# Performance work log

Measured on AMD Instinct MI355X. Metric: run time of the kernel, lower is better.

The kernel has to match this reference:

```python
import jax, jax.numpy as jnp
import numpy as np

FACTOR = 5

def setup_inputs() -> dict:
    key = jax.random.key(0)
    k1, k2, k3 = jax.random.split(key, 3)
    B, L, H, D = 4, 2048, 8, 64
    logL = int(np.ceil(np.log(L)))          # 8
    U_part = min(2 * FACTOR * logL, L)      # 80 sampled keys per query
    queries = jax.random.normal(k1, (B, L, H, D), dtype=jnp.float32)
    keys = jax.random.normal(k2, (B, L, H, D), dtype=jnp.float32)
    index_sample = jax.random.randint(k3, (L, U_part), 0, L)
    return {"queries": queries, "keys": keys, "index_sample": index_sample}

def reference(queries, keys, index_sample):
    B, L, H, D = queries.shape
    q = jnp.transpose(queries, (0, 2, 1, 3))   # [B,H,L,D]
    k = jnp.transpose(keys, (0, 2, 1, 3))      # [B,H,L,D]
    logL = int(np.ceil(np.log(L)))
    u = min(FACTOR * logL, L)                  # n_top queries

    # sample keys per query position: [B,H,L,S,D]
    K_sample = k[:, :, index_sample, :]
    # Q_i . K_sample_ij : [B,H,L,S]
    QK_sample = jnp.einsum('bhld,bhlsd->bhls', q, K_sample)
    # sparsity measure M = max - mean (mean over full L as in source)
    M = QK_sample.max(axis=-1) - QK_sample.sum(axis=-1) / L   # [B,H,L]
    _, M_top = jax.lax.top_k(M, u)                            # [B,H,u]

    # gather selected queries and compute full scores against all keys
    Q_reduce = jnp.take_along_axis(q, M_top[..., None], axis=2)  # [B,H,u,D]
    scale = 1.0 / jnp.sqrt(jnp.float32(D))
    scores = jnp.einsum('bhud,bhld->bhul', Q_reduce, k) * scale  # [B,H,u,L]
    attn = jax.nn.softmax(scores, axis=-1)

    # scatter softmaxed rows into full [B,H,L,L] attention matrix (rest zeros)
    out = jnp.zeros((B, H, L, L), dtype=attn.dtype)
    b_idx = jnp.arange(B)[:, None, None]
    h_idx = jnp.arange(H)[None, :, None]
    out = out.at[b_idx, h_idx, M_top, :].set(attn)
    return out
```

## Files before the change

### kernel.cpp

```cpp
#include <hip/hip_runtime.h>
#include <math.h>

#define NB 4
#define NL 2048
#define NH 8
#define ND 64
#define NUPART 80
#define NUTOP 40

typedef float vfloat4 __attribute__((ext_vector_type(4)));

__global__ __launch_bounds__(256) void k_compute_M(
    const float* __restrict__ q, const float* __restrict__ k,
    const int* __restrict__ idx, float* __restrict__ M)
{
    const int w    = blockIdx.x * 4 + (threadIdx.x >> 6);
    const int lane = threadIdx.x & 63;
    const int l    = w & (NL - 1);
    const int bh   = w >> 11;
    const int h    = bh & (NH - 1);
    const int b    = bh >> 3;
    const int sl   = lane >> 2;
    const int dg   = lane & 3;
    const int d0   = dg * 16;

    const float4* qv = (const float4*)(q + (((size_t)(b * NL + l) * NH + h) * ND + d0));
    const float4 q0 = qv[0], q1 = qv[1], q2 = qv[2], q3 = qv[3];

    float mx = -INFINITY, sm = 0.0f;
#pragma unroll
    for (int r = 0; r < 5; ++r) {
        const int s  = r * 16 + sl;
        const int ki = idx[l * NUPART + s];
        const float4* kv = (const float4*)(k + (((size_t)(b * NL + ki) * NH + h) * ND + d0));
        const float4 k0 = kv[0], k1 = kv[1], k2 = kv[2], k3 = kv[3];
        float p = q0.x * k0.x + q0.y * k0.y + q0.z * k0.z + q0.w * k0.w
                + q1.x * k1.x + q1.y * k1.y + q1.z * k1.z + q1.w * k1.w
                + q2.x * k2.x + q2.y * k2.y + q2.z * k2.z + q2.w * k2.w
                + q3.x * k3.x + q3.y * k3.y + q3.z * k3.z + q3.w * k3.w;
        p += __shfl_xor(p, 1);
        p += __shfl_xor(p, 2);
        mx = fmaxf(mx, p);
        sm += p;
    }
#pragma unroll
    for (int m = 4; m < 64; m <<= 1) {
        mx = fmaxf(mx, __shfl_xor(mx, m));
        sm += __shfl_xor(sm, m);
    }
    if (lane == 0) M[w] = mx - sm * (1.0f / (float)NL);
}

__global__ __launch_bounds__(256) void k_topk(
    const float* __restrict__ M, int* __restrict__ rowmap)
{
    __shared__ float sM[NL];
    __shared__ float rv[4];
    __shared__ int   ri[4];
    const int bh = blockIdx.x;
    const int t  = threadIdx.x;

    for (int j = t; j < NL; j += 256) {
        sM[j] = M[bh * NL + j];
        rowmap[bh * NL + j] = 0;
    }
    __syncthreads();

    for (int it = 0; it < NUTOP; ++it) {
        float v = -INFINITY;
        int   i = NL;
        for (int j = t; j < NL; j += 256) {
            const float m = sM[j];
            if (m > v || (m == v && j < i)) { v = m; i = j; }
        }
#pragma unroll
        for (int off = 1; off < 64; off <<= 1) {
            const float ov = __shfl_xor(v, off);
            const int   oi = __shfl_xor(i, off);
            if (ov > v || (ov == v && oi < i)) { v = ov; i = oi; }
        }
        const int wid = t >> 6;
        if ((t & 63) == 0) { rv[wid] = v; ri[wid] = i; }
        __syncthreads();
        if (t == 0) {
            for (int w2 = 1; w2 < 4; ++w2) {
                if (rv[w2] > v || (rv[w2] == v && ri[w2] < i)) { v = rv[w2]; i = ri[w2]; }
            }
            rowmap[bh * NL + i] = 1;
            sM[i] = -INFINITY;
        }
        __syncthreads();
    }
}

__global__ __launch_bounds__(256) void k_out(
    const float* __restrict__ q, const float* __restrict__ k,
    const int* __restrict__ rowmap, float* __restrict__ out)
{
    const int r   = blockIdx.x;
    const int bh  = r >> 11;
    const int row = r & (NL - 1);
    const int b   = bh >> 3;
    const int h   = bh & 7;
    const int t   = threadIdx.x;

    vfloat4* orow = (vfloat4*)(out + (size_t)r * NL);

    if (!rowmap[r]) {
        const vfloat4 z = (vfloat4)(0.0f);
        __builtin_nontemporal_store(z, orow + t);
        __builtin_nontemporal_store(z, orow + t + 256);
        return;
    }

    __shared__ float redm[4];
    __shared__ float reds[4];
    const int lane = t & 63;
    const int wid  = t >> 6;

    const float4* qv = (const float4*)(q + (((size_t)(b * NL + row)) * NH + h) * ND);
    float4 qr[16];
#pragma unroll
    for (int i = 0; i < 16; ++i) qr[i] = qv[i];

    float sc[8];
    float mx = -INFINITY;
#pragma unroll
    for (int j = 0; j < 8; ++j) {
        const int l = t + 256 * j;
        const float4* kv = (const float4*)(k + (((size_t)(b * NL + l)) * NH + h) * ND);
        float s = 0.0f;
#pragma unroll
        for (int i = 0; i < 16; ++i) {
            const float4 kk = kv[i];
            s += qr[i].x * kk.x + qr[i].y * kk.y + qr[i].z * kk.z + qr[i].w * kk.w;
        }
        sc[j] = s * 0.125f;
        mx = fmaxf(mx, sc[j]);
    }

#pragma unroll
    for (int off = 1; off < 64; off <<= 1) mx = fmaxf(mx, __shfl_xor(mx, off));
    if (lane == 0) redm[wid] = mx;
    __syncthreads();
    mx = fmaxf(fmaxf(redm[0], redm[1]), fmaxf(redm[2], redm[3]));

    float lsum = 0.0f;
#pragma unroll
    for (int j = 0; j < 8; ++j) {
        sc[j] = __expf(sc[j] - mx);
        lsum += sc[j];
    }
#pragma unroll
    for (int off = 1; off < 64; off <<= 1) lsum += __shfl_xor(lsum, off);
    if (lane == 0) reds[wid] = lsum;
    __syncthreads();
    const float inv = 1.0f / (reds[0] + reds[1] + reds[2] + reds[3]);

#pragma unroll
    for (int j = 0; j < 8; ++j) {
        __builtin_nontemporal_store(sc[j] * inv, out + (size_t)r * NL + t + 256 * j);
    }
}

extern "C" void kernel_launch(void* const* d_in, const int* in_sizes, int n_in,
                              void* d_out, int out_size, void* d_ws, size_t ws_size,
                              hipStream_t stream) {
    const float* q   = (const float*)d_in[0];
    const float* k   = (const float*)d_in[1];
    const int*   idx = (const int*)d_in[2];
    float* out = (float*)d_out;

    float* Mws    = (float*)d_ws;
    int*   rowmap = (int*)((char*)d_ws + (size_t)NB * NH * NL * 4);

    k_compute_M<<<NB * NH * NL / 4, 256, 0, stream>>>(q, k, idx, Mws);
    k_topk<<<NB * NH, 256, 0, stream>>>(Mws, rowmap);
    k_out<<<NB * NH * NL, 256, 0, stream>>>(q, k, rowmap, out);
}
```

Before: 413.0 us.

## Fuse all stages into one persistent kernel with grid barriers and overlapped zeroing

Replaces the three launches (sparsity measure, top-k, output) with a single persistent kernel of 512 blocks synchronised by atomic grid barriers. Zeroing of the large output matrix is spread across the phases: it runs alongside the M computation, and idle blocks keep zeroing during the serial top-k on the 32 (batch, head) blocks. The selected attention rows are then computed interleaved with zeroing the remaining rows. The aim is to hide the latency of the launches and of the top-k behind bandwidth-bound zero stores. The cost is barrier spin overhead, a reliance on all blocks being co-resident, and plain stores replacing the earlier nontemporal stores.

Result: slower. 446.5 us (+8.1%).

```diff
diff --git a/kernel.cpp b/kernel.cpp
--- a/kernel.cpp
+++ b/kernel.cpp
@@ -7,159 +7,203 @@
 #define ND 64
 #define NUPART 80
 #define NUTOP 40
+#define NBLK 512
+#define NROWS (NB * NH * NL)
+#define NATTN (NB * NH * NUTOP)
+#define Z1ROWS 20480
+#define Z2ROWS 2048
+#define Z3BASE (Z1ROWS + Z2ROWS)
+#define Z3ROWS (NROWS - Z3BASE)
 
 typedef float vfloat4 __attribute__((ext_vector_type(4)));
 
-__global__ __launch_bounds__(256) void k_compute_M(
+__device__ __forceinline__ void zero_row(float* __restrict__ out, int r, int t) {
+    vfloat4* o = (vfloat4*)out + (size_t)r * (NL / 4) + t;
+    const vfloat4 z = (vfloat4)(0.0f);
+    o[0]   = z;
+    o[256] = z;
+}
+
+__device__ __forceinline__ void gbar(int* cnt, int* gen, int target) {
+    __syncthreads();
+    if (threadIdx.x == 0) {
+        __threadfence();
+        if (atomicAdd(cnt, 1) == NBLK - 1) {
+            atomicExch(cnt, 0);
+            __threadfence();
+            atomicExch(gen, target);
+        } else {
+            while (__hip_atomic_load(gen, __ATOMIC_RELAXED,
+                                     __HIP_MEMORY_SCOPE_AGENT) < target) {
+                __builtin_amdgcn_s_sleep(8);
+            }
+        }
+        __threadfence();
+    }
+    __syncthreads();
+}
+
+__global__ __launch_bounds__(256, 2) void k_fused(
     const float* __restrict__ q, const float* __restrict__ k,
-    const int* __restrict__ idx, float* __restrict__ M)
-{
-    const int w    = blockIdx.x * 4 + (threadIdx.x >> 6);
-    const int lane = threadIdx.x & 63;
-    const int l    = w & (NL - 1);
-    const int bh   = w >> 11;
-    const int h    = bh & (NH - 1);
-    const int b    = bh >> 3;
-    const int sl   = lane >> 2;
-    const int dg   = lane & 3;
-    const int d0   = dg * 16;
-
-    const float4* qv = (const float4*)(q + (((size_t)(b * NL + l) * NH + h) * ND + d0));
-    const float4 q0 = qv[0], q1 = qv[1], q2 = qv[2], q3 = qv[3];
-
-    float mx = -INFINITY, sm = 0.0f;
-#pragma unroll
-    for (int r = 0; r < 5; ++r) {
-        const int s  = r * 16 + sl;
-        const int ki = idx[l * NUPART + s];
-        const float4* kv = (const float4*)(k + (((size_t)(b * NL + ki) * NH + h) * ND + d0));
-        const float4 k0 = kv[0], k1 = kv[1], k2 = kv[2], k3 = kv[3];
-        float p = q0.x * k0.x + q0.y * k0.y + q0.z * k0.z + q0.w * k0.w
-                + q1.x * k1.x + q1.y * k1.y + q1.z * k1.z + q1.w * k1.w
-                + q2.x * k2.x + q2.y * k2.y + q2.z * k2.z + q2.w * k2.w
-                + q3.x * k3.x + q3.y * k3.y + q3.z * k3.z + q3.w * k3.w;
-        p += __shfl_xor(p, 1);
-        p += __shfl_xor(p, 2);
-        mx = fmaxf(mx, p);
-        sm += p;
-    }
-#pragma unroll
-    for (int m = 4; m < 64; m <<= 1) {
-        mx = fmaxf(mx, __shfl_xor(mx, m));
-        sm += __shfl_xor(sm, m);
-    }
-    if (lane == 0) M[w] = mx - sm * (1.0f / (float)NL);
-}
-
-__global__ __launch_bounds__(256) void k_topk(
-    const float* __restrict__ M, int* __restrict__ rowmap)
+    const int* __restrict__ idx, float* __restrict__ M,
+    int* __restrict__ rowmap, int* __restrict__ Mtop,
+    int* __restrict__ bar, float* __restrict__ out)
 {
     __shared__ float sM[NL];
     __shared__ float rv[4];
     __shared__ int   ri[4];
-    const int bh = blockIdx.x;
-    const int t  = threadIdx.x;
-
-    for (int j = t; j < NL; j += 256) {
-        sM[j] = M[bh * NL + j];
-        rowmap[bh * NL + j] = 0;
-    }
-    __syncthreads();
-
-    for (int it = 0; it < NUTOP; ++it) {
-        float v = -INFINITY;
-        int   i = NL;
-        for (int j = t; j < NL; j += 256) {
-            const float m = sM[j];
-            if (m > v || (m == v && j < i)) { v = m; i = j; }
-        }
-#pragma unroll
-        for (int off = 1; off < 64; off <<= 1) {
-            const float ov = __shfl_xor(v, off);
-            const int   oi = __shfl_xor(i, off);
-            if (ov > v || (ov == v && oi < i)) { v = ov; i = oi; }
-        }
-        const int wid = t >> 6;
-        if ((t & 63) == 0) { rv[wid] = v; ri[wid] = i; }
-        __syncthreads();
-        if (t == 0) {
-            for (int w2 = 1; w2 < 4; ++w2) {
-                if (rv[w2] > v || (rv[w2] == v && ri[w2] < i)) { v = rv[w2]; i = ri[w2]; }
-            }
-            rowmap[bh * NL + i] = 1;
-            sM[i] = -INFINITY;
-        }
-        __syncthreads();
-    }
-}
-
-__global__ __launch_bounds__(256) void k_out(
-    const float* __restrict__ q, const float* __restrict__ k,
-    const int* __restrict__ rowmap, float* __restrict__ out)
-{
-    const int r   = blockIdx.x;
-    const int bh  = r >> 11;
-    const int row = r & (NL - 1);
-    const int b   = bh >> 3;
-    const int h   = bh & 7;
-    const int t   = threadIdx.x;
-
-    vfloat4* orow = (vfloat4*)(out + (size_t)r * NL);
-
-    if (!rowmap[r]) {
-        const vfloat4 z = (vfloat4)(0.0f);
-        __builtin_nontemporal_store(z, orow + t);
-        __builtin_nontemporal_store(z, orow + t + 256);
-        return;
-    }
-
     __shared__ float redm[4];
     __shared__ float reds[4];
+
+    const int t    = threadIdx.x;
+    const int bid  = blockIdx.x;
+    const int wid  = t >> 6;
     const int lane = t & 63;
-    const int wid  = t >> 6;
-
-    const float4* qv = (const float4*)(q + (((size_t)(b * NL + row)) * NH + h) * ND);
-    float4 qr[16];
-#pragma unroll
-    for (int i = 0; i < 16; ++i) qr[i] = qv[i];
-
-    float sc[8];
-    float mx = -INFINITY;
-#pragma unroll
-    for (int j = 0; j < 8; ++j) {
-        const int l = t + 256 * j;
-        const float4* kv = (const float4*)(k + (((size_t)(b * NL + l)) * NH + h) * ND);
-        float s = 0.0f;
-#pragma unroll
-        for (int i = 0; i < 16; ++i) {
-            const float4 kk = kv[i];
-            s += qr[i].x * kk.x + qr[i].y * kk.y + qr[i].z * kk.z + qr[i].w * kk.w;
-        }
-        sc[j] = s * 0.125f;
-        mx = fmaxf(mx, sc[j]);
-    }
-
-#pragma unroll
-    for (int off = 1; off < 64; off <<= 1) mx = fmaxf(mx, __shfl_xor(mx, off));
-    if (lane == 0) redm[wid] = mx;
-    __syncthreads();
-    mx = fmaxf(fmaxf(redm[0], redm[1]), fmaxf(redm[2], redm[3]));
-
-    float lsum = 0.0f;
-#pragma unroll
-    for (int j = 0; j < 8; ++j) {
-        sc[j] = __expf(sc[j] - mx);
-        lsum += sc[j];
-    }
-#pragma unroll
-    for (int off = 1; off < 64; off <<= 1) lsum += __shfl_xor(lsum, off);
-    if (lane == 0) reds[wid] = lsum;
-    __syncthreads();
-    const float inv = 1.0f / (reds[0] + reds[1] + reds[2] + reds[3]);
-
-#pragma unroll
-    for (int j = 0; j < 8; ++j) {
-        __builtin_nontemporal_store(sc[j] * inv, out + (size_t)r * NL + t + 256 * j);
+
+    {
+        const int gw = bid * 4 + wid;
+        const int sl = lane >> 2;
+        const int dg = lane & 3;
+        const int d0 = dg * 16;
+
+        for (int j = 0; j < 40; ++j) {
+            if (j < 32) {
+                const int w  = gw + 2048 * j;
+                const int l  = w & (NL - 1);
+                const int bh = w >> 11;
+                const int h  = bh & (NH - 1);
+                const int b  = bh >> 3;
+
+                const float4* qv = (const float4*)(q + (((size_t)(b * NL + l) * NH + h) * ND + d0));
+                const float4 q0 = qv[0], q1 = qv[1], q2 = qv[2], q3 = qv[3];
+
+                float mx = -INFINITY, sm = 0.0f;
+#pragma unroll
+                for (int r = 0; r < 5; ++r) {
+                    const int s  = r * 16 + sl;
+                    const int ki = idx[l * NUPART + s];
+                    const float4* kv = (const float4*)(k + (((size_t)(b * NL + ki) * NH + h) * ND + d0));
+                    const float4 k0 = kv[0], k1 = kv[1], k2 = kv[2], k3 = kv[3];
+                    float p = q0.x * k0.x + q0.y * k0.y + q0.z * k0.z + q0.w * k0.w
+                            + q1.x * k1.x + q1.y * k1.y + q1.z * k1.z + q1.w * k1.w
+                            + q2.x * k2.x + q2.y * k2.y + q2.z * k2.z + q2.w * k2.w
+                            + q3.x * k3.x + q3.y * k3.y + q3.z * k3.z + q3.w * k3.w;
+                    p += __shfl_xor(p, 1);
+                    p += __shfl_xor(p, 2);
+                    mx = fmaxf(mx, p);
+                    sm += p;
+                }
+#pragma unroll
+                for (int m = 4; m < 64; m <<= 1) {
+                    mx = fmaxf(mx, __shfl_xor(mx, m));
+                    sm += __shfl_xor(sm, m);
+                }
+                if (lane == 0) M[w] = mx - sm * (1.0f / (float)NL);
+            }
+            zero_row(out, j * NBLK + bid, t);
+        }
+    }
+
+    gbar(bar, bar + 1, 1);
+
+    if (bid < NB * NH) {
+        const int bh = bid;
+        for (int j = t; j < NL; j += 256) {
+            sM[j] = M[bh * NL + j];
+            rowmap[bh * NL + j] = 0;
+        }
+        __syncthreads();
+
+        for (int it = 0; it < NUTOP; ++it) {
+            float v = -INFINITY;
+            int   i = NL;
+            for (int j = t; j < NL; j += 256) {
+                const float m = sM[j];
+                if (m > v || (m == v && j < i)) { v = m; i = j; }
+            }
+#pragma unroll
+            for (int off = 1; off < 64; off <<= 1) {
+                const float ov = __shfl_xor(v, off);
+                const int   oi = __shfl_xor(i, off);
+                if (ov > v || (ov == v && oi < i)) { v = ov; i = oi; }
+            }
+            if ((t & 63) == 0) { rv[wid] = v; ri[wid] = i; }
+            __syncthreads();
+            if (t == 0) {
+                for (int w2 = 1; w2 < 4; ++w2) {
+                    if (rv[w2] > v || (rv[w2] == v && ri[w2] < i)) { v = rv[w2]; i = ri[w2]; }
+                }
+                Mtop[bh * NUTOP + it] = i;
+                rowmap[bh * NL + i] = 1;
+                sM[i] = -INFINITY;
+            }
+            __syncthreads();
+        }
+    } else {
+        for (int r2 = bid - NB * NH; r2 < Z2ROWS; r2 += NBLK - NB * NH)
+            zero_row(out, Z1ROWS + r2, t);
+    }
+
+    gbar(bar, bar + 1, 2);
+
+    {
+        int a = bid;
+        for (int j = 0; j < Z3ROWS / NBLK; ++j) {
+            if ((j % 28) == 14 && a < NATTN) {
+                const int bh  = a / NUTOP;
+                const int ui  = a % NUTOP;
+                const int b   = bh >> 3;
+                const int h   = bh & 7;
+                const int row = Mtop[bh * NUTOP + ui];
+
+                const float4* qv = (const float4*)(q + (((size_t)(b * NL + row)) * NH + h) * ND);
+                float4 qr[16];
+#pragma unroll
+                for (int i = 0; i < 16; ++i) qr[i] = qv[i];
+
+                float sc[8];
+                float mx = -INFINITY;
+#pragma unroll
+                for (int jj = 0; jj < 8; ++jj) {
+                    const int l = t + 256 * jj;
+                    const float4* kv = (const float4*)(k + (((size_t)(b * NL + l)) * NH + h) * ND);
+                    float s = 0.0f;
+#pragma unroll
+                    for (int i = 0; i < 16; ++i) {
+                        const float4 kk = kv[i];
+                        s += qr[i].x * kk.x + qr[i].y * kk.y + qr[i].z * kk.z + qr[i].w * kk.w;
+                    }
+                    sc[jj] = s * 0.125f;
+                    mx = fmaxf(mx, sc[jj]);
+                }
+#pragma unroll
+                for (int off = 1; off < 64; off <<= 1) mx = fmaxf(mx, __shfl_xor(mx, off));
+                if (lane == 0) redm[wid] = mx;
+                __syncthreads();
+                mx = fmaxf(fmaxf(redm[0], redm[1]), fmaxf(redm[2], redm[3]));
+
+                float lsum = 0.0f;
+#pragma unroll
+                for (int jj = 0; jj < 8; ++jj) {
+                    sc[jj] = __expf(sc[jj] - mx);
+                    lsum += sc[jj];
+                }
+#pragma unroll
+                for (int off = 1; off < 64; off <<= 1) lsum += __shfl_xor(lsum, off);
+                if (lane == 0) reds[wid] = lsum;
+                __syncthreads();
+                const float inv = 1.0f / (reds[0] + reds[1] + reds[2] + reds[3]);
+
+                float* orow = out + ((size_t)bh * NL + row) * NL;
+#pragma unroll
+                for (int jj = 0; jj < 8; ++jj) orow[t + 256 * jj] = sc[jj] * inv;
+
+                a += NBLK;
+                __syncthreads();
+            }
+            const int r = Z3BASE + j * NBLK + bid;
+            if (!rowmap[r]) zero_row(out, r, t);
+        }
     }
 }
 
@@ -172,9 +216,10 @@
     float* out = (float*)d_out;
 
     float* Mws    = (float*)d_ws;
-    int*   rowmap = (int*)((char*)d_ws + (size_t)NB * NH * NL * 4);
-
-    k_compute_M<<<NB * NH * NL / 4, 256, 0, stream>>>(q, k, idx, Mws);
-    k_topk<<<NB * NH, 256, 0, stream>>>(Mws, rowmap);
-    k_out<<<NB * NH * NL, 256, 0, stream>>>(q, k, rowmap, out);
-}
+    int*   rowmap = (int*)((char*)d_ws + (256 << 10));
+    int*   Mtop   = (int*)((char*)d_ws + (512 << 10));
+    int*   bar    = (int*)((char*)d_ws + (520 << 10));
+
+    hipMemsetAsync(bar, 0, 2 * sizeof(int), stream);
+    k_fused<<<NBLK, 256, 0, stream>>>(q, k, idx, Mws, rowmap, Mtop, bar, out);
+}
```
